# Optimization experiments

Hardware: AMD Instinct MI355X
Metric: run time of the kernel (lower is better)

## Reference

```python
import jax, jax.numpy as jnp
import numpy as np

EMBED = 768
HEADS = 6
HEAD_DIM = 256
SEQ = 128
BATCH = 512
EPS = 1e-5


def _layernorm(x, g, b):
    mu = jnp.mean(x, axis=-1, keepdims=True)
    var = jnp.mean(jnp.square(x - mu), axis=-1, keepdims=True)
    return (x - mu) * jax.lax.rsqrt(var + EPS) * g + b


def setup_inputs() -> dict:
    key = jax.random.key(0)
    ks = jax.random.split(key, 10)
    s_in = 1.0 / np.sqrt(EMBED)
    s_cat = 1.0 / np.sqrt(HEADS * HEAD_DIM)
    s_ff = 1.0 / np.sqrt(4 * EMBED)
    return {
        "x": jax.random.normal(ks[0], (BATCH, SEQ, EMBED), jnp.float32),
        # per-head projections (bias=False), stacked over heads: [H, E, D]
        "Wq": jax.random.uniform(ks[1], (HEADS, EMBED, HEAD_DIM), jnp.float32, -s_in, s_in),
        "Wk": jax.random.uniform(ks[2], (HEADS, EMBED, HEAD_DIM), jnp.float32, -s_in, s_in),
        "Wv": jax.random.uniform(ks[3], (HEADS, EMBED, HEAD_DIM), jnp.float32, -s_in, s_in),
        "Wo": jax.random.uniform(ks[4], (HEADS * HEAD_DIM, EMBED), jnp.float32, -s_cat, s_cat),
        "bo": jax.random.uniform(ks[5], (EMBED,), jnp.float32, -s_cat, s_cat),
        "W1": jax.random.uniform(ks[6], (EMBED, 4 * EMBED), jnp.float32, -s_in, s_in),
        "b1": jax.random.uniform(ks[7], (4 * EMBED,), jnp.float32, -s_in, s_in),
        "W2": jax.random.uniform(ks[8], (4 * EMBED, EMBED), jnp.float32, -s_ff, s_ff),
        "b2": jax.random.uniform(ks[9], (EMBED,), jnp.float32, -s_ff, s_ff),
        "g1": jnp.ones((EMBED,), jnp.float32),
        "be1": jnp.zeros((EMBED,), jnp.float32),
        "g2": jnp.ones((EMBED,), jnp.float32),
        "be2": jnp.zeros((EMBED,), jnp.float32),
    }


def reference(x, Wq, Wk, Wv, Wo, bo, W1, b1, W2, b2, g1, be1, g2, be2):
    B, T, E = x.shape
    h = _layernorm(x, g1, be1)
    # per-head projections: [B, H, T, D]
    q = jnp.einsum("bte,hed->bhtd", h, Wq)
    k = jnp.einsum("bte,hed->bhtd", h, Wk)
    v = jnp.einsum("bte,hed->bhtd", h, Wv)
    # NOTE: faithful to source — scale by embed_size**-0.5, not head_size**-0.5
    scores = jnp.einsum("bhtd,bhsd->bhts", q, k) * (E ** -0.5)
    causal = jnp.tril(jnp.ones((T, T), bool))
    scores = jnp.where(causal, scores, -jnp.inf)
    attn = jax.nn.softmax(scores, axis=-1)
    head_out = jnp.einsum("bhts,bhsd->bhtd", attn, v)
    # concat heads in order -> [B, T, H*D]
    cat = head_out.transpose(0, 2, 1, 3).reshape(B, T, HEADS * HEAD_DIM)
    attn_out = cat @ Wo + bo + x
    h2 = _layernorm(attn_out, g2, be2)
    mlp = jax.nn.relu(h2 @ W1 + b1) @ W2 + b2
    return mlp + attn_out
```

## Files before the change

kernel.cpp:

```cpp
#include <hip/hip_runtime.h>
#include <hip/hip_bf16.h>

#define BATCH 512
#define SEQ   128
#define EMB   768
#define NH    6
#define HDIM  256
#define CATD  1536
#define FFD   3072
#define NTOK  (BATCH*SEQ)
#define QKVLD 4608

typedef __attribute__((ext_vector_type(8))) short bfrag;
typedef __attribute__((ext_vector_type(4))) float f32x4;

__device__ __forceinline__ void gld_lds16(const void* g, void* l) {
  __builtin_amdgcn_global_load_lds(
      (const __attribute__((address_space(1))) unsigned int*)g,
      (__attribute__((address_space(3))) unsigned int*)l, 16, 0, 0);
}

__device__ __forceinline__ unsigned short f2bfu(float f) {
  union { __hip_bfloat16 h; unsigned short u; } c;
  c.h = __float2bfloat16(f);
  return c.u;
}

__device__ __forceinline__ void transpose64(const float* in, int C,
                                            __hip_bfloat16* out, int R,
                                            int r0, int c0) {
  __shared__ float tile[64][65];
  const int tx = threadIdx.x & 63;
  const int ty = threadIdx.x >> 6;
#pragma unroll
  for (int i = 0; i < 16; ++i) {
    const int r = ty + i * 4;
    tile[r][tx] = in[(size_t)(r0 + r) * C + c0 + tx];
  }
  __syncthreads();
#pragma unroll
  for (int i = 0; i < 16; ++i) {
    const int cc = ty + i * 4;
    out[(size_t)(c0 + cc) * R + r0 + tx] = __float2bfloat16(tile[tx][cc]);
  }
}

__global__ __launch_bounds__(256) void transpose_cast(const float* __restrict__ in,
                                                      __hip_bfloat16* __restrict__ out,
                                                      int R, int C) {
  transpose64(in, C, out, R, blockIdx.y * 64, blockIdx.x * 64);
}

__global__ __launch_bounds__(256) void repack_qkv(const float* __restrict__ Wq,
                                                  const float* __restrict__ Wk,
                                                  const float* __restrict__ Wv,
                                                  __hip_bfloat16* __restrict__ out) {
  const int z = blockIdx.z, m = z / NH, h = z % NH;
  const float* in = (m == 0 ? Wq : (m == 1 ? Wk : Wv)) + (size_t)h * EMB * HDIM;
  __hip_bfloat16* o = out + (size_t)(m * CATD + h * HDIM) * EMB;
  transpose64(in, HDIM, o, EMB, blockIdx.y * 64, blockIdx.x * 64);
}

__global__ __launch_bounds__(256) void ln_k(const float* __restrict__ src,
                                            const float* __restrict__ gam,
                                            const float* __restrict__ bet,
                                            __hip_bfloat16* __restrict__ dst) {
  const int row = blockIdx.x * 4 + (threadIdx.x >> 6);
  const int l = threadIdx.x & 63;
  const float* x = src + (size_t)row * EMB;
  float4 v[3];
#pragma unroll
  for (int j = 0; j < 3; ++j) v[j] = *(const float4*)(x + j * 256 + l * 4);
  float s = 0.f, ss = 0.f;
#pragma unroll
  for (int j = 0; j < 3; ++j) {
    s  += v[j].x + v[j].y + v[j].z + v[j].w;
    ss += v[j].x * v[j].x + v[j].y * v[j].y + v[j].z * v[j].z + v[j].w * v[j].w;
  }
#pragma unroll
  for (int d = 1; d < 64; d <<= 1) { s += __shfl_xor(s, d, 64); ss += __shfl_xor(ss, d, 64); }
  const float mu = s * (1.f / EMB);
  const float var = ss * (1.f / EMB) - mu * mu;
  const float rs = rsqrtf(var + 1e-5f);
#pragma unroll
  for (int j = 0; j < 3; ++j) {
    float4 g4 = *(const float4*)(gam + j * 256 + l * 4);
    float4 b4 = *(const float4*)(bet + j * 256 + l * 4);
    ushort4 o;
    o.x = f2bfu((v[j].x - mu) * rs * g4.x + b4.x);
    o.y = f2bfu((v[j].y - mu) * rs * g4.y + b4.y);
    o.z = f2bfu((v[j].z - mu) * rs * g4.z + b4.z);
    o.w = f2bfu((v[j].w - mu) * rs * g4.w + b4.w);
    *(ushort4*)((unsigned short*)dst + (size_t)row * EMB + j * 256 + l * 4) = o;
  }
}

template <int MODE>
__global__ __launch_bounds__(256, 2)
void gemm_k(const __hip_bfloat16* __restrict__ A, const __hip_bfloat16* __restrict__ Bt,
            void* __restrict__ Cout, const float* __restrict__ bias,
            const float* __restrict__ res, int M, int N, int K) {
  __shared__ char lds[33792];
  const int tid = threadIdx.x;
  const int w = tid >> 6, l = tid & 63;
  const int l15 = l & 15, lq = l >> 4;
  const int n0 = blockIdx.x * 128, m0 = blockIdx.y * 128;
  const int wm = w >> 1, wn = w & 1;

  const __hip_bfloat16* gsrc[4];
  char* ldst[4];
#pragma unroll
  for (int i = 0; i < 4; ++i) {
    const int c = w * 4 + i;
    const int row = (c < 8) ? (m0 + c * 16 + l15) : (n0 + (c - 8) * 16 + l15);
    const __hip_bfloat16* base = (c < 8) ? A : Bt;
    gsrc[i] = base + (size_t)row * K + lq * 8;
    ldst[i] = lds + c * 1024;
  }

  f32x4 acc[4][4];
#pragma unroll
  for (int i = 0; i < 4; ++i)
#pragma unroll
    for (int j = 0; j < 4; ++j) acc[i][j] = {0.f, 0.f, 0.f, 0.f};

  const int kIters = K >> 5;
#pragma unroll
  for (int i = 0; i < 4; ++i) gld_lds16(gsrc[i], ldst[i]);
#pragma unroll
  for (int i = 0; i < 4; ++i) gsrc[i] += 32;

  for (int kk = 0; kk < kIters; ++kk) {
    if (kk + 1 < kIters) {
      char* nb = lds + ((kk + 1) & 1) * 16384;
#pragma unroll
      for (int i = 0; i < 4; ++i) gld_lds16(gsrc[i], nb + (w * 4 + i) * 1024);
#pragma unroll
      for (int i = 0; i < 4; ++i) gsrc[i] += 32;
      asm volatile("s_waitcnt vmcnt(4)" ::: "memory");
    } else {
      asm volatile("s_waitcnt vmcnt(0)" ::: "memory");
    }
    __builtin_amdgcn_s_barrier();
    const char* cb = lds + (kk & 1) * 16384;
    bfrag af[4], bf[4];
#pragma unroll
    for (int i = 0; i < 4; ++i) {
      af[i] = *(const bfrag*)(cb + ((wm * 4 + i) * 64 + l) * 16);
      bf[i] = *(const bfrag*)(cb + 8192 + ((wn * 4 + i) * 64 + l) * 16);
    }
#pragma unroll
    for (int i = 0; i < 4; ++i)
#pragma unroll
      for (int j = 0; j < 4; ++j)
        acc[i][j] = __builtin_amdgcn_mfma_f32_16x16x32_bf16(af[i], bf[j], acc[i][j], 0, 0, 0);
    __builtin_amdgcn_s_barrier();
  }

  const int cbase = n0 + wn * 64 + l15;
  float bcol[4];
  if (MODE != 0) {
#pragma unroll
    for (int j = 0; j < 4; ++j) bcol[j] = bias[cbase + j * 16];
  }
  for (int p = 0; p < 2; ++p) {
    __syncthreads();
    if (wm == p) {
#pragma unroll
      for (int i = 0; i < 4; ++i)
#pragma unroll
        for (int j = 0; j < 4; ++j)
#pragma unroll
          for (int r = 0; r < 4; ++r) {
            const int lrow = i * 16 + lq * 4 + r;
            const int lcol = wn * 64 + j * 16 + l15;
            float v = acc[i][j][r];
            if (MODE != 0) v += bcol[j];
            if (MODE == 2) v = fmaxf(v, 0.f);
            if (MODE == 1)
              ((float*)lds)[lrow * 132 + lcol] = v;
            else
              ((unsigned short*)lds)[lrow * 136 + lcol] = f2bfu(v);
          }
    }
    __syncthreads();
    if (MODE == 1) {
#pragma unroll
      for (int rep = 0; rep < 8; ++rep) {
        const int lrow = rep * 8 + (tid >> 5);
        const int colf = (tid & 31) * 4;
        float4 v = *(const float4*)((const float*)lds + lrow * 132 + colf);
        const size_t gidx = (size_t)(m0 + p * 64 + lrow) * N + n0 + colf;
        const float4 rv = *(const float4*)(res + gidx);
        v.x += rv.x; v.y += rv.y; v.z += rv.z; v.w += rv.w;
        *(float4*)((float*)Cout + gidx) = v;
      }
    } else {
#pragma unroll
      for (int rep = 0; rep < 4; ++rep) {
        const int lrow = rep * 16 + (tid >> 4);
        const int cols = (tid & 15) * 8;
        const uint4 v = *(const uint4*)((const unsigned short*)lds + lrow * 136 + cols);
        *(uint4*)((__hip_bfloat16*)Cout + (size_t)(m0 + p * 64 + lrow) * N + n0 + cols) = v;
      }
    }
  }
}

__global__ __launch_bounds__(256, 2)
void attn_k(const __hip_bfloat16* __restrict__ qkv, __hip_bfloat16* __restrict__ cat) {
  __shared__ char sm[17408 + 34816 + 2048];
  char* stage = sm;
  unsigned short* P = (unsigned short*)(sm + 17408);
  float* redm = (float*)(sm + 17408 + 34816);
  float* reds = redm + 256;

  const int tid = threadIdx.x;
  const int w = tid >> 6, l = tid & 63;
  const int l15 = l & 15, lq = l >> 4;
  const int wm = w >> 1, wn = w & 1;
  const int bh = blockIdx.x, b = bh / NH, h = bh % NH;
  const unsigned short* qkvu = (const unsigned short*)qkv;
  const size_t tokbase = (size_t)b * SEQ;
  const int qcol = h * HDIM, kcol = CATD + h * HDIM, vcol = 2 * CATD + h * HDIM;

  f32x4 acc[4][4];
#pragma unroll
  for (int i = 0; i < 4; ++i)
#pragma unroll
    for (int j = 0; j < 4; ++j) acc[i][j] = {0.f, 0.f, 0.f, 0.f};

  for (int d0 = 0; d0 < HDIM; d0 += 32) {
#pragma unroll
    for (int i = 0; i < 4; ++i) {
      const int ch = w * 4 + i;
      const int rowloc = (ch & 7) * 16 + l15;
      const int colbase = (ch < 8 ? qcol : kcol) + d0 + lq * 8;
      gld_lds16(qkvu + (tokbase + rowloc) * QKVLD + colbase, stage + ch * 1024);
    }
    __syncthreads();
    bfrag af[4], bf[4];
#pragma unroll
    for (int i = 0; i < 4; ++i) {
      af[i] = *(const bfrag*)(stage + ((wm * 4 + i) * 64 + l) * 16);
      bf[i] = *(const bfrag*)(stage + 8192 + ((wn * 4 + i) * 64 + l) * 16);
    }
#pragma unroll
    for (int i = 0; i < 4; ++i)
#pragma unroll
      for (int j = 0; j < 4; ++j)
        acc[i][j] = __builtin_amdgcn_mfma_f32_16x16x32_bf16(af[i], bf[j], acc[i][j], 0, 0, 0);
    __syncthreads();
  }

  const float scl = 0.03608439182435161f;
  const int rowb = wm * 64 + lq * 4;
  const int colb = wn * 64 + l15;
  float rmax[4][4];
#pragma unroll
  for (int i = 0; i < 4; ++i)
#pragma unroll
    for (int r = 0; r < 4; ++r) {
      const int row = rowb + i * 16 + r;
      float m = -__builtin_inff();
#pragma unroll
      for (int j = 0; j < 4; ++j) {
        const int col = colb + j * 16;
        float sv = acc[i][j][r] * scl;
        if (col > row) sv = -__builtin_inff();
        acc[i][j][r] = sv;
        m = fmaxf(m, sv);
      }
#pragma unroll
      for (int d = 1; d < 16; d <<= 1) m = fmaxf(m, __shfl_xor(m, d, 64));
      rmax[i][r] = m;
    }
  if (l15 == 0) {
#pragma unroll
    for (int i = 0; i < 4; ++i)
#pragma unroll
      for (int r = 0; r < 4; ++r)
        redm[wn * 128 + rowb + i * 16 + r] = rmax[i][r];
  }
  __syncthreads();
  float rsum[4][4];
#pragma unroll
  for (int i = 0; i < 4; ++i)
#pragma unroll
    for (int r = 0; r < 4; ++r) {
      const int row = rowb + i * 16 + r;
      const float mfin = fmaxf(redm[row], redm[128 + row]);
      float sacc = 0.f;
#pragma unroll
      for (int j = 0; j < 4; ++j) {
        float p = __expf(acc[i][j][r] - mfin);
        acc[i][j][r] = p;
        sacc += p;
      }
#pragma unroll
      for (int d = 1; d < 16; d <<= 1) sacc += __shfl_xor(sacc, d, 64);
      rsum[i][r] = sacc;
    }
  if (l15 == 0) {
#pragma unroll
    for (int i = 0; i < 4; ++i)
#pragma unroll
      for (int r = 0; r < 4; ++r)
        reds[wn * 128 + rowb + i * 16 + r] = rsum[i][r];
  }
#pragma unroll
  for (int i = 0; i < 4; ++i)
#pragma unroll
    for (int j = 0; j < 4; ++j)
#pragma unroll
      for (int r = 0; r < 4; ++r)
        P[(rowb + i * 16 + r) * 136 + colb + j * 16] = f2bfu(acc[i][j][r]);
  __syncthreads();

  float invs[4][4];
#pragma unroll
  for (int i = 0; i < 4; ++i)
#pragma unroll
    for (int r = 0; r < 4; ++r) {
      const int row = rowb + i * 16 + r;
      invs[i][r] = 1.f / (reds[row] + reds[128 + row]);
    }

  unsigned short* Vt = (unsigned short*)stage;
  for (int dt = 0; dt < 4; ++dt) {
#pragma unroll
    for (int p4 = 0; p4 < 4; ++p4) {
      const int slot = tid + p4 * 256;
      const int s = slot >> 3, dblk = slot & 7;
      uint4 val = *(const uint4*)(qkvu + (tokbase + s) * QKVLD + vcol + dt * 64 + dblk * 8);
      union { uint4 v; unsigned short u[8]; } uu; uu.v = val;
#pragma unroll
      for (int jj = 0; jj < 8; ++jj) Vt[(dblk * 8 + jj) * 136 + s] = uu.u[jj];
    }
    __syncthreads();
    f32x4 oacc[4][2];
#pragma unroll
    for (int i = 0; i < 4; ++i) { oacc[i][0] = {0.f,0.f,0.f,0.f}; oacc[i][1] = {0.f,0.f,0.f,0.f}; }
#pragma unroll
    for (int ks = 0; ks < 4; ++ks) {
      bfrag pf[4], vf[2];
#pragma unroll
      for (int i = 0; i < 4; ++i)
        pf[i] = *(const bfrag*)((char*)P + ((wm * 64 + i * 16 + l15) * 136 + ks * 32 + lq * 8) * 2);
#pragma unroll
      for (int j = 0; j < 2; ++j)
        vf[j] = *(const bfrag*)((char*)Vt + (((wn * 2 + j) * 16 + l15) * 136 + ks * 32 + lq * 8) * 2);
#pragma unroll
      for (int i = 0; i < 4; ++i)
#pragma unroll
        for (int j = 0; j < 2; ++j)
          oacc[i][j] = __builtin_amdgcn_mfma_f32_16x16x32_bf16(pf[i], vf[j], oacc[i][j], 0, 0, 0);
    }
#pragma unroll
    for (int i = 0; i < 4; ++i)
#pragma unroll
      for (int j = 0; j < 2; ++j)
#pragma unroll
        for (int r = 0; r < 4; ++r) {
          const int trow = rowb + i * 16 + r;
          const int dcol = dt * 64 + wn * 32 + j * 16 + l15;
          cat[(tokbase + trow) * CATD + h * HDIM + dcol] =
              __float2bfloat16(oacc[i][j][r] * invs[i][r]);
        }
    __syncthreads();
  }
}

extern "C" void kernel_launch(void* const* d_in, const int* in_sizes, int n_in,
                              void* d_out, int out_size, void* d_ws, size_t ws_size,
                              hipStream_t stream) {
  const float* x   = (const float*)d_in[0];
  const float* Wq  = (const float*)d_in[1];
  const float* Wk  = (const float*)d_in[2];
  const float* Wv  = (const float*)d_in[3];
  const float* Wo  = (const float*)d_in[4];
  const float* bo  = (const float*)d_in[5];
  const float* W1  = (const float*)d_in[6];
  const float* b1  = (const float*)d_in[7];
  const float* W2  = (const float*)d_in[8];
  const float* b2  = (const float*)d_in[9];
  const float* g1  = (const float*)d_in[10];
  const float* be1 = (const float*)d_in[11];
  const float* g2  = (const float*)d_in[12];
  const float* be2 = (const float*)d_in[13];
  float* out = (float*)d_out;

  const size_t wbytes = (size_t)QKVLD * EMB * 2 + (size_t)EMB * CATD * 2 +
                        (size_t)FFD * EMB * 2 + (size_t)EMB * FFD * 2;
  int nc = 1;
  while (nc < 16 &&
         wbytes + (size_t)(NTOK / nc) * (9216 + 3072 + 3072) + 4096 > ws_size)
    nc <<= 1;
  const int Mc = NTOK / nc;
  const int Bc = BATCH / nc;

  char* ws = (char*)d_ws;
  size_t off = 0;
  auto alloc = [&](size_t bytes) {
    char* p = ws + off;
    off += (bytes + 255) & ~(size_t)255;
    return p;
  };
  __hip_bfloat16* Wqkv_t = (__hip_bfloat16*)alloc((size_t)QKVLD * EMB * 2);
  __hip_bfloat16* Wo_t   = (__hip_bfloat16*)alloc((size_t)EMB * CATD * 2);
  __hip_bfloat16* W1_t   = (__hip_bfloat16*)alloc((size_t)FFD * EMB * 2);
  __hip_bfloat16* W2_t   = (__hip_bfloat16*)alloc((size_t)EMB * FFD * 2);
  char* R1 = (char*)alloc((size_t)Mc * 9216);
  char* R2 = (char*)alloc((size_t)Mc * 3072);
  char* R3 = (char*)alloc((size_t)Mc * 3072);

  repack_qkv<<<dim3(HDIM / 64, EMB / 64, 18), 256, 0, stream>>>(Wq, Wk, Wv, Wqkv_t);
  transpose_cast<<<dim3(EMB / 64, CATD / 64), 256, 0, stream>>>(Wo, Wo_t, CATD, EMB);
  transpose_cast<<<dim3(FFD / 64, EMB / 64), 256, 0, stream>>>(W1, W1_t, EMB, FFD);
  transpose_cast<<<dim3(EMB / 64, FFD / 64), 256, 0, stream>>>(W2, W2_t, FFD, EMB);

  for (int c = 0; c < nc; ++c) {
    const float* xc   = x + (size_t)c * Mc * EMB;
    float*       outc = out + (size_t)c * Mc * EMB;
    __hip_bfloat16* hbuf   = (__hip_bfloat16*)R3;
    __hip_bfloat16* qkv    = (__hip_bfloat16*)R1;
    __hip_bfloat16* cat    = (__hip_bfloat16*)R2;
    float*          attn_o = (float*)R3;
    __hip_bfloat16* h2     = (__hip_bfloat16*)R2;
    __hip_bfloat16* mlp1   = (__hip_bfloat16*)R1;

    ln_k<<<Mc / 4, 256, 0, stream>>>(xc, g1, be1, hbuf);
    gemm_k<0><<<dim3(QKVLD / 128, Mc / 128), 256, 0, stream>>>(
        hbuf, Wqkv_t, qkv, nullptr, nullptr, Mc, QKVLD, EMB);
    attn_k<<<Bc * NH, 256, 0, stream>>>(qkv, cat);
    gemm_k<1><<<dim3(EMB / 128, Mc / 128), 256, 0, stream>>>(
        cat, Wo_t, attn_o, bo, xc, Mc, EMB, CATD);
    ln_k<<<Mc / 4, 256, 0, stream>>>(attn_o, g2, be2, h2);
    gemm_k<2><<<dim3(FFD / 128, Mc / 128), 256, 0, stream>>>(
        h2, W1_t, mlp1, b1, nullptr, Mc, FFD, EMB);
    gemm_k<1><<<dim3(EMB / 128, Mc / 128), 256, 0, stream>>>(
        mlp1, W2_t, outc, b2, attn_o, Mc, EMB, FFD);
  }
}
```

Baseline: 2.968 ms.

## Rewrite GEMM as 256x256 tile, 512-thread kernel with phased LDS pipeline

Replaces the 128x128, 256-thread GEMM with a 256x256 tile computed by 8 waves. It uses a 128 KB LDS double buffer holding a K-step of 64, with global-to-LDS prefetches interleaved between four MFMA phases. It also adds s_setprio around MFMA bursts and an XCD-aware block swizzle. The aim is more operand reuse per loaded byte, fewer barriers per FLOP and better L2 locality. In exchange it has far fewer blocks, and the 128 KB LDS use may limit occupancy to one block per CU. Small tail-wave effects are possible on the N=768 GEMMs.

```diff
diff --git a/kernel.cpp b/kernel.cpp
--- a/kernel.cpp
+++ b/kernel.cpp
@@ -95,117 +95,181 @@
   }
 }
 
+#define PHASE(S, MH) do {                                                    \
+    bfrag af[4], bv[4];                                                      \
+    const char* Ab = cbuf + ((S)*16 + wm*8 + (MH)*4) * 1024 + l * 16;        \
+    const char* Bb = cbuf + 32768 + ((S)*16 + wn*4) * 1024 + l * 16;         \
+    _Pragma("unroll")                                                        \
+    for (int i = 0; i < 4; ++i) af[i] = *(const bfrag*)(Ab + i * 1024);      \
+    _Pragma("unroll")                                                        \
+    for (int n = 0; n < 4; ++n) bv[n] = *(const bfrag*)(Bb + n * 1024);      \
+    __builtin_amdgcn_s_setprio(1);                                          \
+    _Pragma("unroll")                                                        \
+    for (int i = 0; i < 4; ++i)                                              \
+      _Pragma("unroll")                                                      \
+      for (int n = 0; n < 4; ++n)                                            \
+        acc[(MH)*4 + i][n] = __builtin_amdgcn_mfma_f32_16x16x32_bf16(        \
+            af[i], bv[n], acc[(MH)*4 + i][n], 0, 0, 0);                      \
+    __builtin_amdgcn_s_setprio(0);                                          \
+  } while (0)
+
+#define PH_END                                                \
+  asm volatile("s_waitcnt lgkmcnt(0)" ::: "memory");          \
+  asm volatile("s_barrier" ::: "memory")
+
+#define STG(p, koff, dstoff) gld_lds16((p) + (koff), lds + (dstoff))
+
 template <int MODE>
-__global__ __launch_bounds__(256, 2)
+__global__ __launch_bounds__(512, 2)
 void gemm_k(const __hip_bfloat16* __restrict__ A, const __hip_bfloat16* __restrict__ Bt,
             void* __restrict__ Cout, const float* __restrict__ bias,
             const float* __restrict__ res, int M, int N, int K) {
-  __shared__ char lds[33792];
+  __shared__ char lds[131072];
   const int tid = threadIdx.x;
   const int w = tid >> 6, l = tid & 63;
   const int l15 = l & 15, lq = l >> 4;
-  const int n0 = blockIdx.x * 128, m0 = blockIdx.y * 128;
-  const int wm = w >> 1, wn = w & 1;
-
-  const __hip_bfloat16* gsrc[4];
-  char* ldst[4];
-#pragma unroll
-  for (int i = 0; i < 4; ++i) {
-    const int c = w * 4 + i;
-    const int row = (c < 8) ? (m0 + c * 16 + l15) : (n0 + (c - 8) * 16 + l15);
-    const __hip_bfloat16* base = (c < 8) ? A : Bt;
-    gsrc[i] = base + (size_t)row * K + lq * 8;
-    ldst[i] = lds + c * 1024;
-  }
-
-  f32x4 acc[4][4];
-#pragma unroll
-  for (int i = 0; i < 4; ++i)
-#pragma unroll
-    for (int j = 0; j < 4; ++j) acc[i][j] = {0.f, 0.f, 0.f, 0.f};
-
-  const int kIters = K >> 5;
-#pragma unroll
-  for (int i = 0; i < 4; ++i) gld_lds16(gsrc[i], ldst[i]);
-#pragma unroll
-  for (int i = 0; i < 4; ++i) gsrc[i] += 32;
-
-  for (int kk = 0; kk < kIters; ++kk) {
-    if (kk + 1 < kIters) {
-      char* nb = lds + ((kk + 1) & 1) * 16384;
-#pragma unroll
-      for (int i = 0; i < 4; ++i) gld_lds16(gsrc[i], nb + (w * 4 + i) * 1024);
-#pragma unroll
-      for (int i = 0; i < 4; ++i) gsrc[i] += 32;
-      asm volatile("s_waitcnt vmcnt(4)" ::: "memory");
+  const int wm = w >> 2, wn = w & 3;
+
+  const int nwg = gridDim.x * gridDim.y;
+  const int orig = blockIdx.y * gridDim.x + blockIdx.x;
+  const int cpx = nwg >> 3;
+  const int sw = (orig & 7) * cpx + (orig >> 3);
+  const int n0 = (sw % gridDim.x) * 256;
+  const int m0 = (sw / gridDim.x) * 256;
+
+  const unsigned short* Au = (const unsigned short*)A;
+  const unsigned short* Bu = (const unsigned short*)Bt;
+  const unsigned short* pA_lo = Au + (size_t)(m0 + w * 16 + l15) * K + lq * 8;
+  const unsigned short* pA_hi = Au + (size_t)(m0 + 128 + w * 16 + l15) * K + lq * 8;
+  const unsigned short* pB_lo = Bu + (size_t)(n0 + w * 16 + l15) * K + lq * 8;
+  const unsigned short* pB_hi = Bu + (size_t)(n0 + 128 + w * 16 + l15) * K + lq * 8;
+
+  f32x4 acc[8][4];
+#pragma unroll
+  for (int i = 0; i < 8; ++i)
+#pragma unroll
+    for (int n = 0; n < 4; ++n) acc[i][n] = {0.f, 0.f, 0.f, 0.f};
+
+  const int kIters = K >> 6;
+
+  STG(pA_lo, 0,  (0 + w) * 1024);
+  STG(pA_hi, 0,  (8 + w) * 1024);
+  STG(pB_lo, 0,  32768 + (0 + w) * 1024);
+  STG(pB_hi, 0,  32768 + (8 + w) * 1024);
+  STG(pA_lo, 32, (16 + w) * 1024);
+  STG(pA_hi, 32, (24 + w) * 1024);
+  STG(pB_lo, 32, 32768 + (16 + w) * 1024);
+  STG(pB_hi, 32, 32768 + (24 + w) * 1024);
+  STG(pA_lo, 64, 65536 + (0 + w) * 1024);
+  STG(pA_hi, 64, 65536 + (8 + w) * 1024);
+  STG(pB_lo, 64, 65536 + 32768 + (0 + w) * 1024);
+  STG(pB_hi, 64, 65536 + 32768 + (8 + w) * 1024);
+
+  for (int kt = 0; kt < kIters; ++kt) {
+    const int cOff = (kt & 1) * 65536;
+    const int nOff = cOff ^ 65536;
+    const char* cbuf = lds + cOff;
+    const bool pre1 = (kt + 1 < kIters);
+    const bool pre2 = (kt + 2 < kIters);
+    const int k1 = (kt + 1) * 64 + 32;
+    const int k2 = (kt + 2) * 64;
+
+    if (pre1) {
+      STG(pA_lo, k1, nOff + (16 + w) * 1024);
+      STG(pB_lo, k1, nOff + 32768 + (16 + w) * 1024);
+      asm volatile("s_waitcnt vmcnt(6)" ::: "memory");
     } else {
       asm volatile("s_waitcnt vmcnt(0)" ::: "memory");
     }
-    __builtin_amdgcn_s_barrier();
-    const char* cb = lds + (kk & 1) * 16384;
-    bfrag af[4], bf[4];
-#pragma unroll
-    for (int i = 0; i < 4; ++i) {
-      af[i] = *(const bfrag*)(cb + ((wm * 4 + i) * 64 + l) * 16);
-      bf[i] = *(const bfrag*)(cb + 8192 + ((wn * 4 + i) * 64 + l) * 16);
-    }
-#pragma unroll
-    for (int i = 0; i < 4; ++i)
-#pragma unroll
-      for (int j = 0; j < 4; ++j)
-        acc[i][j] = __builtin_amdgcn_mfma_f32_16x16x32_bf16(af[i], bf[j], acc[i][j], 0, 0, 0);
-    __builtin_amdgcn_s_barrier();
-  }
-
-  const int cbase = n0 + wn * 64 + l15;
+    asm volatile("s_barrier" ::: "memory");
+    PHASE(0, 0);
+    PH_END;
+    if (pre1) {
+      STG(pA_hi, k1, nOff + (24 + w) * 1024);
+      STG(pB_hi, k1, nOff + 32768 + (24 + w) * 1024);
+    }
+    PHASE(0, 1);
+    PH_END;
+    if (pre2) {
+      STG(pA_lo, k2, cOff + (0 + w) * 1024);
+      STG(pB_lo, k2, cOff + 32768 + (0 + w) * 1024);
+    }
+    PHASE(1, 0);
+    PH_END;
+    if (pre2) {
+      STG(pA_hi, k2, cOff + (8 + w) * 1024);
+      STG(pB_hi, k2, cOff + 32768 + (8 + w) * 1024);
+    }
+    PHASE(1, 1);
+    PH_END;
+  }
+
   float bcol[4];
   if (MODE != 0) {
 #pragma unroll
-    for (int j = 0; j < 4; ++j) bcol[j] = bias[cbase + j * 16];
-  }
-  for (int p = 0; p < 2; ++p) {
-    __syncthreads();
-    if (wm == p) {
-#pragma unroll
-      for (int i = 0; i < 4; ++i)
-#pragma unroll
-        for (int j = 0; j < 4; ++j)
-#pragma unroll
-          for (int r = 0; r < 4; ++r) {
-            const int lrow = i * 16 + lq * 4 + r;
-            const int lcol = wn * 64 + j * 16 + l15;
-            float v = acc[i][j][r];
-            if (MODE != 0) v += bcol[j];
-            if (MODE == 2) v = fmaxf(v, 0.f);
-            if (MODE == 1)
-              ((float*)lds)[lrow * 132 + lcol] = v;
-            else
-              ((unsigned short*)lds)[lrow * 136 + lcol] = f2bfu(v);
-          }
-    }
-    __syncthreads();
-    if (MODE == 1) {
+    for (int n = 0; n < 4; ++n) bcol[n] = bias[n0 + wn * 64 + n * 16 + l15];
+  }
+  if (MODE == 1) {
+#pragma unroll
+    for (int q = 0; q < 4; ++q) {
+      if (q) __syncthreads();
+      if (wm == (q >> 1)) {
+#pragma unroll
+        for (int i2 = 0; i2 < 4; ++i2)
+#pragma unroll
+          for (int n = 0; n < 4; ++n)
+#pragma unroll
+            for (int r = 0; r < 4; ++r) {
+              const int lrow = i2 * 16 + lq * 4 + r;
+              const int col = wn * 64 + n * 16 + l15;
+              ((float*)lds)[lrow * 260 + col] = acc[(q & 1) * 4 + i2][n][r] + bcol[n];
+            }
+      }
+      __syncthreads();
 #pragma unroll
       for (int rep = 0; rep < 8; ++rep) {
-        const int lrow = rep * 8 + (tid >> 5);
-        const int colf = (tid & 31) * 4;
-        float4 v = *(const float4*)((const float*)lds + lrow * 132 + colf);
-        const size_t gidx = (size_t)(m0 + p * 64 + lrow) * N + n0 + colf;
+        const int row = rep * 8 + (tid >> 6);
+        const int colf = (tid & 63) * 4;
+        float4 v = *(const float4*)((const float*)lds + row * 260 + colf);
+        const size_t gidx = (size_t)(m0 + q * 64 + row) * N + n0 + colf;
         const float4 rv = *(const float4*)(res + gidx);
         v.x += rv.x; v.y += rv.y; v.z += rv.z; v.w += rv.w;
         *(float4*)((float*)Cout + gidx) = v;
       }
-    } else {
-#pragma unroll
-      for (int rep = 0; rep < 4; ++rep) {
-        const int lrow = rep * 16 + (tid >> 4);
-        const int cols = (tid & 15) * 8;
-        const uint4 v = *(const uint4*)((const unsigned short*)lds + lrow * 136 + cols);
-        *(uint4*)((__hip_bfloat16*)Cout + (size_t)(m0 + p * 64 + lrow) * N + n0 + cols) = v;
+    }
+  } else {
+#pragma unroll
+    for (int p = 0; p < 2; ++p) {
+      if (p) __syncthreads();
+      if (wm == p) {
+#pragma unroll
+        for (int i = 0; i < 8; ++i)
+#pragma unroll
+          for (int n = 0; n < 4; ++n)
+#pragma unroll
+            for (int r = 0; r < 4; ++r) {
+              const int lrow = i * 16 + lq * 4 + r;
+              const int col = wn * 64 + n * 16 + l15;
+              float v = acc[i][n][r];
+              if (MODE == 2) v = fmaxf(v + bcol[n], 0.f);
+              ((unsigned short*)lds)[lrow * 264 + col] = f2bfu(v);
+            }
       }
-    }
-  }
-}
+      __syncthreads();
+#pragma unroll
+      for (int rep = 0; rep < 8; ++rep) {
+        const int row = rep * 16 + (tid >> 5);
+        const int colc = (tid & 31) * 8;
+        const uint4 v = *(const uint4*)((const unsigned short*)lds + row * 264 + colc);
+        *(uint4*)((__hip_bfloat16*)Cout + (size_t)(m0 + p * 128 + row) * N + n0 + colc) = v;
+      }
+    }
+  }
+}
+
+#undef PHASE
+#undef PH_END
+#undef STG
 
 __global__ __launch_bounds__(256, 2)
 void attn_k(const __hip_bfloat16* __restrict__ qkv, __hip_bfloat16* __restrict__ cat) {
@@ -430,15 +494,15 @@
     __hip_bfloat16* mlp1   = (__hip_bfloat16*)R1;
 
     ln_k<<<Mc / 4, 256, 0, stream>>>(xc, g1, be1, hbuf);
-    gemm_k<0><<<dim3(QKVLD / 128, Mc / 128), 256, 0, stream>>>(
+    gemm_k<0><<<dim3(QKVLD / 256, Mc / 256), 512, 0, stream>>>(
         hbuf, Wqkv_t, qkv, nullptr, nullptr, Mc, QKVLD, EMB);
     attn_k<<<Bc * NH, 256, 0, stream>>>(qkv, cat);
-    gemm_k<1><<<dim3(EMB / 128, Mc / 128), 256, 0, stream>>>(
+    gemm_k<1><<<dim3(EMB / 256, Mc / 256), 512, 0, stream>>>(
         cat, Wo_t, attn_o, bo, xc, Mc, EMB, CATD);
     ln_k<<<Mc / 4, 256, 0, stream>>>(attn_o, g2, be2, h2);
-    gemm_k<2><<<dim3(FFD / 128, Mc / 128), 256, 0, stream>>>(
+    gemm_k<2><<<dim3(FFD / 256, Mc / 256), 512, 0, stream>>>(
         h2, W1_t, mlp1, b1, nullptr, Mc, FFD, EMB);
-    gemm_k<1><<<dim3(EMB / 128, Mc / 128), 256, 0, stream>>>(
+    gemm_k<1><<<dim3(EMB / 256, Mc / 256), 512, 0, stream>>>(
         mlp1, W2_t, outc, b2, attn_o, Mc, EMB, FFD);
   }
 }
```

After: 2.429 ms. 18.1% less time.
